# Performance work log

Hardware: AMD Instinct MI355X
Metric: run time of the kernel (lower is better)

## Reference

```python
import math
import jax, jax.numpy as jnp
import numpy as np

B, T, N, D, H = 4, 12, 512, 256, 8


def _xavier(key, shape):
    limit = math.sqrt(6.0 / (shape[0] + shape[1]))
    return jax.random.uniform(key, shape, jnp.float32, -limit, limit)


def setup_inputs() -> dict:
    key = jax.random.key(0)
    kx, ks, kq, kk, kv, ko = jax.random.split(key, 6)
    return {
        "x": jax.random.normal(kx, (B, T, N, D), jnp.float32),
        "sim": jax.random.normal(ks, (N, N), jnp.float32),
        "Wq": _xavier(kq, (D, D)),
        "Wk": _xavier(kk, (D, D)),
        "Wv": _xavier(kv, (D, D)),
        "Wo": _xavier(ko, (D, D)),
    }


def reference(x, sim, Wq, Wk, Wv, Wo):
    # x: [B, T, N, D]; attention over spatial dim N, per (batch, time, head).
    b, t, n, d = x.shape
    hd = d // H
    scale = 1.0 / math.sqrt(hd)

    def split_heads(z):  # [B,T,N,D] -> [B,H,T,N,hd]
        return z.reshape(b, t, n, H, hd).transpose(0, 3, 1, 2, 4)

    q = split_heads(x @ Wq)
    k = split_heads(x @ Wk)
    v = split_heads(x @ Wv)

    # scores: [B,H,T,N,N]; additive sim bias broadcast over B,H,T
    scores = jnp.einsum("bhtnd,bhtmd->bhtnm", q, k) * scale + sim
    attn = jax.nn.softmax(scores, axis=-1)  # (dropout p=0.1 omitted: eval mode)
    out = jnp.einsum("bhtnm,bhtmd->bhtnd", attn, v)
    out = out.transpose(0, 2, 3, 1, 4).reshape(b, t, n, d)  # merge heads
    return out @ Wo
```

## Files before the change

### kernel.cpp

```cpp
#include <hip/hip_runtime.h>
#include <hip/hip_bf16.h>

#define BTT 48
#define SEQ 512
#define DIM 256
#define NH  8
#define HD  32
#define QKVD 768

typedef unsigned short u16;
typedef __attribute__((ext_vector_type(8))) short bf16x8;
typedef __attribute__((ext_vector_type(4))) float f32x4;
typedef __attribute__((ext_vector_type(2))) unsigned int u32x2;

__device__ __forceinline__ float fexp2(float x) {
#if __has_builtin(__builtin_amdgcn_exp2f)
  return __builtin_amdgcn_exp2f(x);
#else
  float r; asm("v_exp_f32 %0, %1" : "=v"(r) : "v"(x)); return r;
#endif
}
__device__ __forceinline__ unsigned cvtpk_bf16(float lo, float hi) {
  unsigned r;
  asm("v_cvt_pk_bf16_f32 %0, %1, %2" : "=v"(r) : "v"(lo), "v"(hi));
  return r;
}

__device__ __forceinline__ u16 f2b(float f) {
  __hip_bfloat16 h = __float2bfloat16(f);
  union { __hip_bfloat16 h; u16 u; } c; c.h = h; return c.u;
}
__device__ __forceinline__ bf16x8 ldfrag8(const u16* p) {
  union { uint2 u[2]; bf16x8 v; } f;
  f.u[0] = *reinterpret_cast<const uint2*>(p);
  f.u[1] = *reinterpret_cast<const uint2*>(p + 4);
  return f.v;
}
__device__ __forceinline__ bf16x8 ldfrag16(const u16* p) {
  union { uint4 u; bf16x8 v; } f;
  f.u = *reinterpret_cast<const uint4*>(p);
  return f.v;
}

__global__ __launch_bounds__(256) void prep_kernel(const float* __restrict__ W0,
                                                   const float* __restrict__ W1,
                                                   const float* __restrict__ W2,
                                                   const float* __restrict__ W3,
                                                   const float* __restrict__ sim,
                                                   u16* __restrict__ dst,
                                                   float* __restrict__ simT2,
                                                   float sc0) {
  __shared__ float Ls[64][65];
  const int z = blockIdx.z;
  const int t = threadIdx.x;
  if (z == 4) {
    const float LOG2E = 1.4426950408889634f;
    const int b = blockIdx.x * 4 + blockIdx.y;
#pragma unroll
    for (int i = 0; i < 16; ++i) {
      int gid = b * 4096 + i * 256 + t;
      int q = gid & 511, k4 = gid >> 9;
      float4 v = *reinterpret_cast<const float4*>(&sim[(size_t)q * 512 + k4 * 4]);
      v.x *= LOG2E; v.y *= LOG2E; v.z *= LOG2E; v.w *= LOG2E;
      *reinterpret_cast<float4*>(&simT2[((size_t)k4 * 512 + q) * 4]) = v;
    }
    return;
  }
  const float* W = (z == 0) ? W0 : (z == 1) ? W1 : (z == 2) ? W2 : W3;
  u16* Bt = dst + (size_t)z * DIM * DIM;
  const float sc = (z == 0) ? sc0 : 1.0f;
  const int kt = blockIdx.x * 64, nt = blockIdx.y * 64;
#pragma unroll
  for (int it = 0; it < 4; ++it) {
    int r = (t >> 4) + it * 16;
    int c = (t & 15) * 4;
    float4 v = *reinterpret_cast<const float4*>(&W[(size_t)(kt + r) * 256 + nt + c]);
    Ls[r][c] = v.x; Ls[r][c + 1] = v.y; Ls[r][c + 2] = v.z; Ls[r][c + 3] = v.w;
  }
  __syncthreads();
  const int n = t >> 2, kc = (t & 3) * 16;
  union { uint4 u[2]; u16 s[16]; } ob;
#pragma unroll
  for (int j = 0; j < 16; ++j) ob.s[j] = f2b(Ls[kc + j][n] * sc);
  u16* dp = Bt + (size_t)(nt + n) * 256 + kt + kc;
  *reinterpret_cast<uint4*>(dp)     = ob.u[0];
  *reinterpret_cast<uint4*>(dp + 8) = ob.u[1];
}

template <typename AIN, typename OUT>
__global__ __launch_bounds__(256) void gemm_mfma(const AIN* __restrict__ A,
                                                 const u16* __restrict__ Bt,
                                                 OUT* __restrict__ C,
                                                 int M, int N, int K) {
  __shared__ u16 As[128][36];
  __shared__ u16 Bs[128][36];
  const int t = threadIdx.x, lane = t & 63, w = t >> 6;
  const int g = lane >> 4, ln = lane & 15;

  const int gx = gridDim.x, gy = gridDim.y;
  const int flat = blockIdx.x + gx * blockIdx.y;
  const int chunk = (gx * gy) >> 3;
  const int work = (flat & 7) * chunk + (flat >> 3);
  const int bm = (work / gy) * 128, bn = (work % gy) * 128;

  const int wr = (w & 1) * 64, wc = (w >> 1) * 64;
  const f32x4 zf = {0.f, 0.f, 0.f, 0.f};
  f32x4 acc[4][4];
#pragma unroll
  for (int i = 0; i < 4; ++i)
#pragma unroll
    for (int j = 0; j < 4; ++j) acc[i][j] = zf;

  const int r0 = t >> 2, c8 = (t & 3) * 8;
  uint4 bpre[2];
  float4 apf0[2], apf1[2];
  uint4 apb[2];
#pragma unroll
  for (int p = 0; p < 2; ++p) {
    const size_t arow = (size_t)(bm + r0 + p * 64) * K + c8;
    if constexpr (sizeof(AIN) == 4) {
      apf0[p] = *reinterpret_cast<const float4*>((const float*)A + arow);
      apf1[p] = *reinterpret_cast<const float4*>((const float*)A + arow + 4);
    } else {
      apb[p] = *reinterpret_cast<const uint4*>((const u16*)A + arow);
    }
    bpre[p] = *reinterpret_cast<const uint4*>(&Bt[(size_t)(bn + r0 + p * 64) * K + c8]);
  }

  for (int k0 = 0; k0 < K; k0 += 32) {
#pragma unroll
    for (int p = 0; p < 2; ++p) {
      const int r = r0 + p * 64;
      uint2 a0, a1;
      if constexpr (sizeof(AIN) == 4) {
        a0.x = cvtpk_bf16(apf0[p].x, apf0[p].y);
        a0.y = cvtpk_bf16(apf0[p].z, apf0[p].w);
        a1.x = cvtpk_bf16(apf1[p].x, apf1[p].y);
        a1.y = cvtpk_bf16(apf1[p].z, apf1[p].w);
      } else {
        union { uint4 u4; uint2 u2[2]; } av; av.u4 = apb[p];
        a0 = av.u2[0]; a1 = av.u2[1];
      }
      union { uint4 u4; uint2 u2[2]; } bv; bv.u4 = bpre[p];
      *reinterpret_cast<uint2*>(&As[r][c8])     = a0;
      *reinterpret_cast<uint2*>(&As[r][c8 + 4]) = a1;
      *reinterpret_cast<uint2*>(&Bs[r][c8])     = bv.u2[0];
      *reinterpret_cast<uint2*>(&Bs[r][c8 + 4]) = bv.u2[1];
    }
    if (k0 + 32 < K) {
#pragma unroll
      for (int p = 0; p < 2; ++p) {
        const size_t arow = (size_t)(bm + r0 + p * 64) * K + k0 + 32 + c8;
        if constexpr (sizeof(AIN) == 4) {
          apf0[p] = *reinterpret_cast<const float4*>((const float*)A + arow);
          apf1[p] = *reinterpret_cast<const float4*>((const float*)A + arow + 4);
        } else {
          apb[p] = *reinterpret_cast<const uint4*>((const u16*)A + arow);
        }
        bpre[p] = *reinterpret_cast<const uint4*>(&Bt[(size_t)(bn + r0 + p * 64) * K + k0 + 32 + c8]);
      }
    }
    __syncthreads();
    bf16x8 af[4], bfr[4];
#pragma unroll
    for (int i = 0; i < 4; ++i) af[i]  = ldfrag8(&As[wr + i * 16 + ln][g * 8]);
#pragma unroll
    for (int j = 0; j < 4; ++j) bfr[j] = ldfrag8(&Bs[wc + j * 16 + ln][g * 8]);
#pragma unroll
    for (int i = 0; i < 4; ++i)
#pragma unroll
      for (int j = 0; j < 4; ++j)
        acc[i][j] = __builtin_amdgcn_mfma_f32_16x16x32_bf16(af[i], bfr[j], acc[i][j], 0, 0, 0);
    __syncthreads();
  }
#pragma unroll
  for (int i = 0; i < 4; ++i)
#pragma unroll
    for (int j = 0; j < 4; ++j)
#pragma unroll
      for (int r = 0; r < 4; ++r) {
        const int row = bm + wr + i * 16 + g * 4 + r;
        const int col = bn + wc + j * 16 + ln;
        if constexpr (sizeof(OUT) == 2)
          ((u16*)C)[(size_t)row * N + col] = f2b(acc[i][j][r]);
        else
          ((float*)C)[(size_t)row * N + col] = acc[i][j][r];
      }
}

#define TRRD(dst, base, OFFSTR) \
  asm volatile("ds_read_b64_tr_b16 %0, %1 offset:" OFFSTR : "=v"(dst) : "v"(base))

__global__ __launch_bounds__(256) void attn_mfma14(const u16* __restrict__ QKV,
                                                   const float* __restrict__ simT2,
                                                   u16* __restrict__ O) {
  __shared__ u16 Ks[2][64][36];
  __shared__ u16 Vn[2][2][64][16];
  __shared__ u16 Pws[4][2][16][68];

  const int t = threadIdx.x;
  const int lane = t & 63, w = t >> 6;
  const int g = lane >> 4, ln = lane & 15;

  const int flat = blockIdx.x + 4 * (blockIdx.y + 8 * (int)blockIdx.z);
  const int work = (flat & 7) * 192 + (flat >> 3);
  const int qb = work & 3;
  const int grp = work >> 2;
  const int h = grp & 7, bt = grp >> 3;

  const size_t base = (size_t)bt * SEQ * QKVD + (size_t)h * HD;
  const u16* Qp = QKV + base;
  const u16* Kp = QKV + base + 256;
  const u16* Vp = QKV + base + 512;
  const size_t baseo = (size_t)bt * SEQ * DIM + (size_t)h * HD;
  const int wq = qb * 128 + w * 32;

  bf16x8 qf[2];
#pragma unroll
  for (int qt = 0; qt < 2; ++qt)
    qf[qt] = ldfrag16(&Qp[(size_t)(wq + qt * 16 + ln) * QKVD + g * 8]);

  const f32x4 zf = {0.f, 0.f, 0.f, 0.f};
  f32x4 o[2][2];
  float lacc[2];
#pragma unroll
  for (int qt = 0; qt < 2; ++qt) { o[qt][0] = zf; o[qt][1] = zf; lacc[qt] = 0.f; }

  const float4* bq[2];
#pragma unroll
  for (int qt = 0; qt < 2; ++qt)
    bq[qt] = (const float4*)simT2 + ((size_t)g * 512 + (wq + qt * 16 + ln));

  const int sr = t >> 2, sc8 = (t & 3) * 8;
  uint4 kreg = *reinterpret_cast<const uint4*>(&Kp[(size_t)sr * QKVD + sc8]);
  uint4 vreg = *reinterpret_cast<const uint4*>(&Vp[(size_t)sr * QKVD + sc8]);

  const unsigned trbase0 = (unsigned)(unsigned long long)(&Vn[0][0][0][0])
                         + (unsigned)(g * 256 + ln * 8);

  for (int it = 0; it < 8; ++it) {
    const int buf = it & 1;
    {
      union { uint4 u4; uint2 u2[2]; } kv;
      kv.u4 = kreg;
      *reinterpret_cast<uint2*>(&Ks[buf][sr][sc8])     = kv.u2[0];
      *reinterpret_cast<uint2*>(&Ks[buf][sr][sc8 + 4]) = kv.u2[1];
      *reinterpret_cast<uint4*>(&Vn[buf][sc8 >> 4][sr][sc8 & 15]) = vreg;
    }
    if (it < 7) {
      const size_t off = (size_t)(it + 1) * 64 * QKVD + (size_t)sr * QKVD + sc8;
      kreg = *reinterpret_cast<const uint4*>(&Kp[off]);
      vreg = *reinterpret_cast<const uint4*>(&Vp[off]);
    }
    __syncthreads();

    float4 bc[2][4];
#pragma unroll
    for (int qt = 0; qt < 2; ++qt)
#pragma unroll
      for (int kt = 0; kt < 4; ++kt)
        bc[qt][kt] = bq[qt][kt * 2048];

    bf16x8 kf[4];
#pragma unroll
    for (int kt = 0; kt < 4; ++kt) kf[kt] = ldfrag8(&Ks[buf][kt * 16 + ln][g * 8]);

    bf16x8 vf[2][2];
    {
      const unsigned trb = trbase0 + (unsigned)(buf * 4096);
      u32x2 r00a, r00b, r01a, r01b, r10a, r10b, r11a, r11b;
      TRRD(r00a, trb, "0");     TRRD(r00b, trb, "128");
      TRRD(r01a, trb, "1024");  TRRD(r01b, trb, "1152");
      TRRD(r10a, trb, "2048");  TRRD(r10b, trb, "2176");
      TRRD(r11a, trb, "3072");  TRRD(r11b, trb, "3200");
      asm volatile("s_waitcnt lgkmcnt(0)" ::: "memory");
      __builtin_amdgcn_sched_barrier(0);
      union { u32x2 p[2]; bf16x8 v; } u;
      u.p[0] = r00a; u.p[1] = r00b; vf[0][0] = u.v;
      u.p[0] = r01a; u.p[1] = r01b; vf[0][1] = u.v;
      u.p[0] = r10a; u.p[1] = r10b; vf[1][0] = u.v;
      u.p[0] = r11a; u.p[1] = r11b; vf[1][1] = u.v;
    }

#pragma unroll
    for (int qt = 0; qt < 2; ++qt) {
      f32x4 s[4];
#pragma unroll
      for (int kt = 0; kt < 4; ++kt) {
        const float4 b4 = bc[qt][kt];
        f32x4 ci = {b4.x, b4.y, b4.z, b4.w};
        s[kt] = ci;
      }
      __builtin_amdgcn_s_setprio(1);
#pragma unroll
      for (int kt = 0; kt < 4; ++kt)
        s[kt] = __builtin_amdgcn_mfma_f32_16x16x32_bf16(kf[kt], qf[qt], s[kt], 0, 0, 0);
      __builtin_amdgcn_s_setprio(0);
      bf16x8 pfr[2];
      if (qt > 0) {
#pragma unroll
        for (int ks = 0; ks < 2; ++ks)
          pfr[ks] = ldfrag8(&Pws[w][0][ln][ks * 32 + g * 8]);
      }
      float lsum = 0.f;
#pragma unroll
      for (int kt = 0; kt < 4; ++kt) {
        const float e0 = fexp2(s[kt][0]);
        const float e1 = fexp2(s[kt][1]);
        const float e2 = fexp2(s[kt][2]);
        const float e3 = fexp2(s[kt][3]);
        lsum += (e0 + e1) + (e2 + e3);
        uint2 pw;
        pw.x = cvtpk_bf16(e0, e1);
        pw.y = cvtpk_bf16(e2, e3);
        *reinterpret_cast<uint2*>(&Pws[w][qt][ln][kt * 16 + g * 4]) = pw;
      }
      __builtin_amdgcn_sched_barrier(0);
      lacc[qt] += lsum;
      if (qt > 0) {
        __builtin_amdgcn_s_setprio(1);
#pragma unroll
        for (int ks = 0; ks < 2; ++ks)
#pragma unroll
          for (int hf = 0; hf < 2; ++hf)
            o[0][hf] = __builtin_amdgcn_mfma_f32_16x16x32_bf16(pfr[ks], vf[hf][ks], o[0][hf], 0, 0, 0);
        __builtin_amdgcn_s_setprio(0);
      }
    }
    {
      bf16x8 pfr[2];
#pragma unroll
      for (int ks = 0; ks < 2; ++ks)
        pfr[ks] = ldfrag8(&Pws[w][1][ln][ks * 32 + g * 8]);
      __builtin_amdgcn_s_setprio(1);
#pragma unroll
      for (int ks = 0; ks < 2; ++ks)
#pragma unroll
        for (int hf = 0; hf < 2; ++hf)
          o[1][hf] = __builtin_amdgcn_mfma_f32_16x16x32_bf16(pfr[ks], vf[hf][ks], o[1][hf], 0, 0, 0);
      __builtin_amdgcn_s_setprio(0);
    }
#pragma unroll
    for (int qt = 0; qt < 2; ++qt) bq[qt] += 16 * 512;
  }

#pragma unroll
  for (int qt = 0; qt < 2; ++qt) {
    float l = lacc[qt];
    l += __shfl_xor(l, 16);
    l += __shfl_xor(l, 32);
    const float invl = 1.0f / l;
#pragma unroll
    for (int r = 0; r < 4; ++r) {
      const float il = __shfl(invl, g * 4 + r);
      const int qrow = wq + qt * 16 + g * 4 + r;
      O[baseo + (size_t)qrow * DIM + ln]      = f2b(o[qt][0][r] * il);
      O[baseo + (size_t)qrow * DIM + 16 + ln] = f2b(o[qt][1][r] * il);
    }
  }
}

extern "C" void kernel_launch(void* const* d_in, const int* in_sizes, int n_in,
                              void* d_out, int out_size, void* d_ws, size_t ws_size,
                              hipStream_t stream) {
  const float* x   = (const float*)d_in[0];
  const float* sim = (const float*)d_in[1];
  const float* Wq  = (const float*)d_in[2];
  const float* Wk  = (const float*)d_in[3];
  const float* Wv  = (const float*)d_in[4];
  const float* Wo  = (const float*)d_in[5];
  float* out = (float*)d_out;

  const int M = BTT * SEQ;
  const size_t sz = (size_t)M * DIM;
  const int WN = DIM * DIM;
  const float SCALE2 = 0.17677669529663687f * 1.4426950408889634f;

  u16* QKVw  = (u16*)d_ws;
  u16* Aw    = QKVw + (size_t)M * QKVD;
  u16* Wqkvb = Aw + sz;
  u16* Wob   = Wqkvb + (size_t)3 * WN;
  float* simT2 = (float*)(Wob + WN);

  prep_kernel<<<dim3(4, 4, 5), 256, 0, stream>>>(Wq, Wk, Wv, Wo, sim, Wqkvb, simT2, SCALE2);

  gemm_mfma<float, u16><<<dim3(M / 128, QKVD / 128), 256, 0, stream>>>(x, Wqkvb, QKVw, M, QKVD, DIM);

  attn_mfma14<<<dim3(4, NH, BTT), 256, 0, stream>>>(QKVw, simT2, Aw);

  gemm_mfma<u16, float><<<dim3(M / 128, DIM / 128), 256, 0, stream>>>(Aw, Wob, out, M, DIM, DIM);
}
```

Before: 77.97 us.

## Compute softmax row sums via MFMA with ones, reorder attention, use 128x64 output GEMM

After: 75.92 us (median of 4 runs). 2.6% less time.

```diff
diff --git a/kernel.cpp b/kernel.cpp
--- a/kernel.cpp
+++ b/kernel.cpp
@@ -87,11 +87,10 @@
   *reinterpret_cast<uint4*>(dp + 8) = ob.u[1];
 }
 
-template <typename AIN, typename OUT>
-__global__ __launch_bounds__(256) void gemm_mfma(const AIN* __restrict__ A,
-                                                 const u16* __restrict__ Bt,
-                                                 OUT* __restrict__ C,
-                                                 int M, int N, int K) {
+__global__ __launch_bounds__(256) void gemm_qkv(const float* __restrict__ A,
+                                                const u16* __restrict__ Bt,
+                                                u16* __restrict__ C,
+                                                int M, int N, int K) {
   __shared__ u16 As[128][36];
   __shared__ u16 Bs[128][36];
   const int t = threadIdx.x, lane = t & 63, w = t >> 6;
@@ -114,16 +113,11 @@
   const int r0 = t >> 2, c8 = (t & 3) * 8;
   uint4 bpre[2];
   float4 apf0[2], apf1[2];
-  uint4 apb[2];
 #pragma unroll
   for (int p = 0; p < 2; ++p) {
     const size_t arow = (size_t)(bm + r0 + p * 64) * K + c8;
-    if constexpr (sizeof(AIN) == 4) {
-      apf0[p] = *reinterpret_cast<const float4*>((const float*)A + arow);
-      apf1[p] = *reinterpret_cast<const float4*>((const float*)A + arow + 4);
-    } else {
-      apb[p] = *reinterpret_cast<const uint4*>((const u16*)A + arow);
-    }
+    apf0[p] = *reinterpret_cast<const float4*>(A + arow);
+    apf1[p] = *reinterpret_cast<const float4*>(A + arow + 4);
     bpre[p] = *reinterpret_cast<const uint4*>(&Bt[(size_t)(bn + r0 + p * 64) * K + c8]);
   }
 
@@ -132,15 +126,10 @@
     for (int p = 0; p < 2; ++p) {
       const int r = r0 + p * 64;
       uint2 a0, a1;
-      if constexpr (sizeof(AIN) == 4) {
-        a0.x = cvtpk_bf16(apf0[p].x, apf0[p].y);
-        a0.y = cvtpk_bf16(apf0[p].z, apf0[p].w);
-        a1.x = cvtpk_bf16(apf1[p].x, apf1[p].y);
-        a1.y = cvtpk_bf16(apf1[p].z, apf1[p].w);
-      } else {
-        union { uint4 u4; uint2 u2[2]; } av; av.u4 = apb[p];
-        a0 = av.u2[0]; a1 = av.u2[1];
-      }
+      a0.x = cvtpk_bf16(apf0[p].x, apf0[p].y);
+      a0.y = cvtpk_bf16(apf0[p].z, apf0[p].w);
+      a1.x = cvtpk_bf16(apf1[p].x, apf1[p].y);
+      a1.y = cvtpk_bf16(apf1[p].z, apf1[p].w);
       union { uint4 u4; uint2 u2[2]; } bv; bv.u4 = bpre[p];
       *reinterpret_cast<uint2*>(&As[r][c8])     = a0;
       *reinterpret_cast<uint2*>(&As[r][c8 + 4]) = a1;
@@ -151,12 +140,8 @@
 #pragma unroll
       for (int p = 0; p < 2; ++p) {
         const size_t arow = (size_t)(bm + r0 + p * 64) * K + k0 + 32 + c8;
-        if constexpr (sizeof(AIN) == 4) {
-          apf0[p] = *reinterpret_cast<const float4*>((const float*)A + arow);
-          apf1[p] = *reinterpret_cast<const float4*>((const float*)A + arow + 4);
-        } else {
-          apb[p] = *reinterpret_cast<const uint4*>((const u16*)A + arow);
-        }
+        apf0[p] = *reinterpret_cast<const float4*>(A + arow);
+        apf1[p] = *reinterpret_cast<const float4*>(A + arow + 4);
         bpre[p] = *reinterpret_cast<const uint4*>(&Bt[(size_t)(bn + r0 + p * 64) * K + k0 + 32 + c8]);
       }
     }
@@ -181,17 +166,109 @@
       for (int r = 0; r < 4; ++r) {
         const int row = bm + wr + i * 16 + g * 4 + r;
         const int col = bn + wc + j * 16 + ln;
-        if constexpr (sizeof(OUT) == 2)
-          ((u16*)C)[(size_t)row * N + col] = f2b(acc[i][j][r]);
-        else
-          ((float*)C)[(size_t)row * N + col] = acc[i][j][r];
+        C[(size_t)row * N + col] = f2b(acc[i][j][r]);
+      }
+}
+
+__global__ __launch_bounds__(256) void gemm_o64(const u16* __restrict__ A,
+                                                const u16* __restrict__ Bt,
+                                                float* __restrict__ C,
+                                                int M, int N, int K) {
+  __shared__ u16 As[2][128][36];
+  __shared__ u16 Bs[2][64][36];
+  const int t = threadIdx.x, lane = t & 63, w = t >> 6;
+  const int g = lane >> 4, ln = lane & 15;
+
+  const int gx = gridDim.x, gy = gridDim.y;
+  const int flat = blockIdx.x + gx * blockIdx.y;
+  const int chunk = (gx * gy) >> 3;
+  const int work = (flat & 7) * chunk + (flat >> 3);
+  const int bm = (work / gy) * 128, bn = (work % gy) * 64;
+
+  const int wr = (w & 1) * 64, wc = (w >> 1) * 32;
+  const f32x4 zf = {0.f, 0.f, 0.f, 0.f};
+  f32x4 acc[4][2];
+#pragma unroll
+  for (int i = 0; i < 4; ++i) { acc[i][0] = zf; acc[i][1] = zf; }
+
+  const int ra = t >> 2, ca = t & 3;
+  const int ch = ca >> 1, co = (ca & 1) * 16;
+  uint4 apre[2][2], bpre[2];
+#pragma unroll
+  for (int p = 0; p < 2; ++p) {
+    const size_t arow = (size_t)(bm + ra + p * 64) * K + ca * 16;
+    apre[p][0] = *reinterpret_cast<const uint4*>(A + arow);
+    apre[p][1] = *reinterpret_cast<const uint4*>(A + arow + 8);
+  }
+  {
+    const size_t brow = (size_t)(bn + ra) * K + ca * 16;
+    bpre[0] = *reinterpret_cast<const uint4*>(Bt + brow);
+    bpre[1] = *reinterpret_cast<const uint4*>(Bt + brow + 8);
+  }
+
+  for (int k0 = 0; k0 < K; k0 += 64) {
+#pragma unroll
+    for (int p = 0; p < 2; ++p) {
+      u16* dst = &As[ch][ra + p * 64][co];
+      union { uint4 u4; uint2 u2[2]; } v0, v1;
+      v0.u4 = apre[p][0]; v1.u4 = apre[p][1];
+      *reinterpret_cast<uint2*>(dst)      = v0.u2[0];
+      *reinterpret_cast<uint2*>(dst + 4)  = v0.u2[1];
+      *reinterpret_cast<uint2*>(dst + 8)  = v1.u2[0];
+      *reinterpret_cast<uint2*>(dst + 12) = v1.u2[1];
+    }
+    {
+      u16* dst = &Bs[ch][ra][co];
+      union { uint4 u4; uint2 u2[2]; } v0, v1;
+      v0.u4 = bpre[0]; v1.u4 = bpre[1];
+      *reinterpret_cast<uint2*>(dst)      = v0.u2[0];
+      *reinterpret_cast<uint2*>(dst + 4)  = v0.u2[1];
+      *reinterpret_cast<uint2*>(dst + 8)  = v1.u2[0];
+      *reinterpret_cast<uint2*>(dst + 12) = v1.u2[1];
+    }
+    if (k0 + 64 < K) {
+#pragma unroll
+      for (int p = 0; p < 2; ++p) {
+        const size_t arow = (size_t)(bm + ra + p * 64) * K + k0 + 64 + ca * 16;
+        apre[p][0] = *reinterpret_cast<const uint4*>(A + arow);
+        apre[p][1] = *reinterpret_cast<const uint4*>(A + arow + 8);
+      }
+      const size_t brow = (size_t)(bn + ra) * K + k0 + 64 + ca * 16;
+      bpre[0] = *reinterpret_cast<const uint4*>(Bt + brow);
+      bpre[1] = *reinterpret_cast<const uint4*>(Bt + brow + 8);
+    }
+    __syncthreads();
+#pragma unroll
+    for (int kk = 0; kk < 2; ++kk) {
+      bf16x8 af[4], bfr[2];
+#pragma unroll
+      for (int i = 0; i < 4; ++i) af[i]  = ldfrag8(&As[kk][wr + i * 16 + ln][g * 8]);
+#pragma unroll
+      for (int j = 0; j < 2; ++j) bfr[j] = ldfrag8(&Bs[kk][wc + j * 16 + ln][g * 8]);
+#pragma unroll
+      for (int i = 0; i < 4; ++i)
+#pragma unroll
+        for (int j = 0; j < 2; ++j)
+          acc[i][j] = __builtin_amdgcn_mfma_f32_16x16x32_bf16(af[i], bfr[j], acc[i][j], 0, 0, 0);
+    }
+    __syncthreads();
+  }
+#pragma unroll
+  for (int i = 0; i < 4; ++i)
+#pragma unroll
+    for (int j = 0; j < 2; ++j)
+#pragma unroll
+      for (int r = 0; r < 4; ++r) {
+        const int row = bm + wr + i * 16 + g * 4 + r;
+        const int col = bn + wc + j * 16 + ln;
+        C[(size_t)row * N + col] = acc[i][j][r];
       }
 }
 
 #define TRRD(dst, base, OFFSTR) \
   asm volatile("ds_read_b64_tr_b16 %0, %1 offset:" OFFSTR : "=v"(dst) : "v"(base))
 
-__global__ __launch_bounds__(256) void attn_mfma14(const u16* __restrict__ QKV,
+__global__ __launch_bounds__(256) void attn_mfma16(const u16* __restrict__ QKV,
                                                    const float* __restrict__ simT2,
                                                    u16* __restrict__ O) {
   __shared__ u16 Ks[2][64][36];
@@ -220,11 +297,13 @@
   for (int qt = 0; qt < 2; ++qt)
     qf[qt] = ldfrag16(&Qp[(size_t)(wq + qt * 16 + ln) * QKVD + g * 8]);
 
+  const short oneb = (short)0x3F80;
+  const bf16x8 onesf = {oneb, oneb, oneb, oneb, oneb, oneb, oneb, oneb};
+
   const f32x4 zf = {0.f, 0.f, 0.f, 0.f};
-  f32x4 o[2][2];
-  float lacc[2];
-#pragma unroll
-  for (int qt = 0; qt < 2; ++qt) { o[qt][0] = zf; o[qt][1] = zf; lacc[qt] = 0.f; }
+  f32x4 o[2][2], o_l[2];
+#pragma unroll
+  for (int qt = 0; qt < 2; ++qt) { o[qt][0] = zf; o[qt][1] = zf; o_l[qt] = zf; }
 
   const float4* bq[2];
 #pragma unroll
@@ -265,16 +344,69 @@
 #pragma unroll
     for (int kt = 0; kt < 4; ++kt) kf[kt] = ldfrag8(&Ks[buf][kt * 16 + ln][g * 8]);
 
-    bf16x8 vf[2][2];
+    u32x2 r00a, r00b, r01a, r01b, r10a, r10b, r11a, r11b;
     {
       const unsigned trb = trbase0 + (unsigned)(buf * 4096);
-      u32x2 r00a, r00b, r01a, r01b, r10a, r10b, r11a, r11b;
       TRRD(r00a, trb, "0");     TRRD(r00b, trb, "128");
       TRRD(r01a, trb, "1024");  TRRD(r01b, trb, "1152");
       TRRD(r10a, trb, "2048");  TRRD(r10b, trb, "2176");
       TRRD(r11a, trb, "3072");  TRRD(r11b, trb, "3200");
-      asm volatile("s_waitcnt lgkmcnt(0)" ::: "memory");
+    }
+
+    {
+      f32x4 s[4];
+#pragma unroll
+      for (int kt = 0; kt < 4; ++kt) {
+        const float4 b4 = bc[0][kt];
+        f32x4 ci = {b4.x, b4.y, b4.z, b4.w};
+        s[kt] = ci;
+      }
+      __builtin_amdgcn_s_setprio(1);
+#pragma unroll
+      for (int kt = 0; kt < 4; ++kt)
+        s[kt] = __builtin_amdgcn_mfma_f32_16x16x32_bf16(kf[kt], qf[0], s[kt], 0, 0, 0);
+      __builtin_amdgcn_s_setprio(0);
+#pragma unroll
+      for (int kt = 0; kt < 4; ++kt) {
+        uint2 pw;
+        pw.x = cvtpk_bf16(fexp2(s[kt][0]), fexp2(s[kt][1]));
+        pw.y = cvtpk_bf16(fexp2(s[kt][2]), fexp2(s[kt][3]));
+        *reinterpret_cast<uint2*>(&Pws[w][0][ln][kt * 16 + g * 4]) = pw;
+      }
       __builtin_amdgcn_sched_barrier(0);
+    }
+
+    bf16x8 pfr0[2];
+    {
+      f32x4 s[4];
+#pragma unroll
+      for (int kt = 0; kt < 4; ++kt) {
+        const float4 b4 = bc[1][kt];
+        f32x4 ci = {b4.x, b4.y, b4.z, b4.w};
+        s[kt] = ci;
+      }
+      __builtin_amdgcn_s_setprio(1);
+#pragma unroll
+      for (int kt = 0; kt < 4; ++kt)
+        s[kt] = __builtin_amdgcn_mfma_f32_16x16x32_bf16(kf[kt], qf[1], s[kt], 0, 0, 0);
+      __builtin_amdgcn_s_setprio(0);
+#pragma unroll
+      for (int ks = 0; ks < 2; ++ks)
+        pfr0[ks] = ldfrag8(&Pws[w][0][ln][ks * 32 + g * 8]);
+#pragma unroll
+      for (int kt = 0; kt < 4; ++kt) {
+        uint2 pw;
+        pw.x = cvtpk_bf16(fexp2(s[kt][0]), fexp2(s[kt][1]));
+        pw.y = cvtpk_bf16(fexp2(s[kt][2]), fexp2(s[kt][3]));
+        *reinterpret_cast<uint2*>(&Pws[w][1][ln][kt * 16 + g * 4]) = pw;
+      }
+      __builtin_amdgcn_sched_barrier(0);
+    }
+
+    asm volatile("s_waitcnt lgkmcnt(0)" ::: "memory");
+    __builtin_amdgcn_sched_barrier(0);
+    bf16x8 vf[2][2];
+    {
       union { u32x2 p[2]; bf16x8 v; } u;
       u.p[0] = r00a; u.p[1] = r00b; vf[0][0] = u.v;
       u.p[0] = r01a; u.p[1] = r01b; vf[0][1] = u.v;
@@ -282,82 +414,44 @@
       u.p[0] = r11a; u.p[1] = r11b; vf[1][1] = u.v;
     }
 
-#pragma unroll
-    for (int qt = 0; qt < 2; ++qt) {
-      f32x4 s[4];
-#pragma unroll
-      for (int kt = 0; kt < 4; ++kt) {
-        const float4 b4 = bc[qt][kt];
-        f32x4 ci = {b4.x, b4.y, b4.z, b4.w};
-        s[kt] = ci;
-      }
+    __builtin_amdgcn_s_setprio(1);
+#pragma unroll
+    for (int ks = 0; ks < 2; ++ks) {
+#pragma unroll
+      for (int hf = 0; hf < 2; ++hf)
+        o[0][hf] = __builtin_amdgcn_mfma_f32_16x16x32_bf16(pfr0[ks], vf[hf][ks], o[0][hf], 0, 0, 0);
+      o_l[0] = __builtin_amdgcn_mfma_f32_16x16x32_bf16(pfr0[ks], onesf, o_l[0], 0, 0, 0);
+    }
+    __builtin_amdgcn_s_setprio(0);
+
+    {
+      bf16x8 pfr1[2];
+#pragma unroll
+      for (int ks = 0; ks < 2; ++ks)
+        pfr1[ks] = ldfrag8(&Pws[w][1][ln][ks * 32 + g * 8]);
       __builtin_amdgcn_s_setprio(1);
 #pragma unroll
-      for (int kt = 0; kt < 4; ++kt)
-        s[kt] = __builtin_amdgcn_mfma_f32_16x16x32_bf16(kf[kt], qf[qt], s[kt], 0, 0, 0);
+      for (int ks = 0; ks < 2; ++ks) {
+#pragma unroll
+        for (int hf = 0; hf < 2; ++hf)
+          o[1][hf] = __builtin_amdgcn_mfma_f32_16x16x32_bf16(pfr1[ks], vf[hf][ks], o[1][hf], 0, 0, 0);
+        o_l[1] = __builtin_amdgcn_mfma_f32_16x16x32_bf16(pfr1[ks], onesf, o_l[1], 0, 0, 0);
+      }
       __builtin_amdgcn_s_setprio(0);
-      bf16x8 pfr[2];
-      if (qt > 0) {
-#pragma unroll
-        for (int ks = 0; ks < 2; ++ks)
-          pfr[ks] = ldfrag8(&Pws[w][0][ln][ks * 32 + g * 8]);
-      }
-      float lsum = 0.f;
-#pragma unroll
-      for (int kt = 0; kt < 4; ++kt) {
-        const float e0 = fexp2(s[kt][0]);
-        const float e1 = fexp2(s[kt][1]);
-        const float e2 = fexp2(s[kt][2]);
-        const float e3 = fexp2(s[kt][3]);
-        lsum += (e0 + e1) + (e2 + e3);
-        uint2 pw;
-        pw.x = cvtpk_bf16(e0, e1);
-        pw.y = cvtpk_bf16(e2, e3);
-        *reinterpret_cast<uint2*>(&Pws[w][qt][ln][kt * 16 + g * 4]) = pw;
-      }
-      __builtin_amdgcn_sched_barrier(0);
-      lacc[qt] += lsum;
-      if (qt > 0) {
-        __builtin_amdgcn_s_setprio(1);
-#pragma unroll
-        for (int ks = 0; ks < 2; ++ks)
-#pragma unroll
-          for (int hf = 0; hf < 2; ++hf)
-            o[0][hf] = __builtin_amdgcn_mfma_f32_16x16x32_bf16(pfr[ks], vf[hf][ks], o[0][hf], 0, 0, 0);
-        __builtin_amdgcn_s_setprio(0);
-      }
-    }
-    {
-      bf16x8 pfr[2];
-#pragma unroll
-      for (int ks = 0; ks < 2; ++ks)
-        pfr[ks] = ldfrag8(&Pws[w][1][ln][ks * 32 + g * 8]);
-      __builtin_amdgcn_s_setprio(1);
-#pragma unroll
-      for (int ks = 0; ks < 2; ++ks)
-#pragma unroll
-        for (int hf = 0; hf < 2; ++hf)
-          o[1][hf] = __builtin_amdgcn_mfma_f32_16x16x32_bf16(pfr[ks], vf[hf][ks], o[1][hf], 0, 0, 0);
-      __builtin_amdgcn_s_setprio(0);
     }
 #pragma unroll
     for (int qt = 0; qt < 2; ++qt) bq[qt] += 16 * 512;
   }
 
 #pragma unroll
-  for (int qt = 0; qt < 2; ++qt) {
-    float l = lacc[qt];
-    l += __shfl_xor(l, 16);
-    l += __shfl_xor(l, 32);
-    const float invl = 1.0f / l;
+  for (int qt = 0; qt < 2; ++qt)
 #pragma unroll
     for (int r = 0; r < 4; ++r) {
-      const float il = __shfl(invl, g * 4 + r);
+      const float il = 1.0f / o_l[qt][r];
       const int qrow = wq + qt * 16 + g * 4 + r;
       O[baseo + (size_t)qrow * DIM + ln]      = f2b(o[qt][0][r] * il);
       O[baseo + (size_t)qrow * DIM + 16 + ln] = f2b(o[qt][1][r] * il);
     }
-  }
 }
 
 extern "C" void kernel_launch(void* const* d_in, const int* in_sizes, int n_in,
@@ -384,9 +478,9 @@
 
   prep_kernel<<<dim3(4, 4, 5), 256, 0, stream>>>(Wq, Wk, Wv, Wo, sim, Wqkvb, simT2, SCALE2);
 
-  gemm_mfma<float, u16><<<dim3(M / 128, QKVD / 128), 256, 0, stream>>>(x, Wqkvb, QKVw, M, QKVD, DIM);
-
-  attn_mfma14<<<dim3(4, NH, BTT), 256, 0, stream>>>(QKVw, simT2, Aw);
-
-  gemm_mfma<u16, float><<<dim3(M / 128, DIM / 128), 256, 0, stream>>>(Aw, Wob, out, M, DIM, DIM);
-}
+  gemm_qkv<<<dim3(M / 128, QKVD / 128), 256, 0, stream>>>(x, Wqkvb, QKVw, M, QKVD, DIM);
+
+  attn_mfma16<<<dim3(4, NH, BTT), 256, 0, stream>>>(QKVw, simT2, Aw);
+
+  gemm_o64<<<dim3(M / 128, DIM / 64), 256, 0, stream>>>(Aw, Wob, out, M, DIM, DIM);
+}
```
